# Kernel tuning notes

Measured on AMD Instinct MI355X. Metric: run time of the kernel, lower is better.

Reference implementation:

```python
import jax, jax.numpy as jnp
import numpy as np

H = 16  # number of heads (init kwarg h)

def vdp_matmul(a, va, b, vb):
    # VDP propagation through a matmul of two independent Gaussian tensors:
    # mean = a @ b ; var = va @ vb + va @ b^2 + a^2 @ vb
    mu = jnp.matmul(a, b)
    var = jnp.matmul(va, vb) + jnp.matmul(va, b * b) + jnp.matmul(a * a, vb)
    return mu, var

def softmax_vdp(a, va):
    # diagonal-Jacobian VDP softmax: p = softmax(a); var = (p(1-p))^2 * va
    p = jax.nn.softmax(a, axis=-1)
    return p, (p * (1.0 - p)) ** 2 * va

def setup_inputs() -> dict:
    key = jax.random.key(0)
    ks = jax.random.split(key, 8)
    B, S, D = 2, 1024, 1024
    sc = 1.0 / np.sqrt(D)
    return {
        "x": jax.random.normal(ks[0], (B, S, D), jnp.float32),
        "var_x": jax.random.uniform(ks[1], (B, S, D), jnp.float32) * 0.1,
        "wq_mu": jax.random.normal(ks[2], (D, D), jnp.float32) * sc,
        "wq_var": jax.random.uniform(ks[3], (D, D), jnp.float32) * 0.01,
        "wk_mu": jax.random.normal(ks[4], (D, D), jnp.float32) * sc,
        "wk_var": jax.random.uniform(ks[5], (D, D), jnp.float32) * 0.01,
        "wv_mu": jax.random.normal(ks[6], (D, D), jnp.float32) * sc,
        "wv_var": jax.random.uniform(ks[7], (D, D), jnp.float32) * 0.01,
    }

def _split_heads(t, h):
    B, S, D = t.shape
    return t.reshape(B, S, h, D // h).transpose(0, 2, 1, 3)  # [B,h,S,dh]

def reference(x, var_x, wq_mu, wq_var, wk_mu, wk_var, wv_mu, wv_var):
    D = x.shape[-1]
    rd = jnp.sqrt(jnp.asarray(D, x.dtype))
    # LinearVDP (bias=False): treat weight^T as the second VDP matmul operand
    q, vq = vdp_matmul(x, var_x, wq_mu.T, wq_var.T)
    k, vk = vdp_matmul(x, var_x, wk_mu.T, wk_var.T)
    v, vv = vdp_matmul(x, var_x, wv_mu.T, wv_var.T)
    q, vq = _split_heads(q, H), _split_heads(vq, H)
    k, vk = _split_heads(k, H), _split_heads(vk, H)
    v, vv = _split_heads(v, H), _split_heads(vv, H)
    # scores: q @ k^T with VDP variance, scaled (masking=False path)
    a, va = vdp_matmul(q, vq, k.transpose(0, 1, 3, 2), vk.transpose(0, 1, 3, 2))
    a, va = a / rd, va / (rd * rd)
    a, va = softmax_vdp(a, va)
    # attention-weighted values with VDP variance
    a, va = vdp_matmul(a, va, v, vv)
    a = a.transpose(0, 2, 1, 3).reshape(x.shape)      # [B,S,D]
    va = va.transpose(0, 2, 1, 3).reshape(x.shape)    # [B,S,D]
    return x + a, va
```

## Files before the change

### kernel.cpp

```cpp
#include <hip/hip_runtime.h>
#include <stdint.h>

typedef unsigned short u16;
typedef __attribute__((ext_vector_type(4))) float f32x4;
typedef __attribute__((ext_vector_type(8))) short s16x8;
typedef __attribute__((ext_vector_type(2))) unsigned u32x2;

#define MFMA16(a,b,c) __builtin_amdgcn_mfma_f32_16x16x32_bf16(a,b,c,0,0,0)

__device__ inline u16 f2b(float f){
  unsigned u = __float_as_uint(f);
  unsigned r = u + 0x7fffu + ((u>>16)&1u);
  return (u16)(r>>16);
}
__device__ inline float b2f(u16 b){
  return __uint_as_float(((unsigned)b)<<16);
}
__device__ inline unsigned cvtpk(float lo, float hi){
  unsigned r;
  asm("v_cvt_pk_bf16_f32 %0, %1, %2" : "=v"(r) : "v"(lo), "v"(hi));
  return r;
}
__device__ inline void load_lds16(const void* g, void* l){
  __builtin_amdgcn_global_load_lds((const __attribute__((address_space(1))) void*)g,
                                   (__attribute__((address_space(3))) void*)l, 16, 0, 0);
}

__global__ void prep_in_kernel(const float* __restrict__ x, const float* __restrict__ vx,
                               const float* __restrict__ w0mu, const float* __restrict__ w0va,
                               const float* __restrict__ w1mu, const float* __restrict__ w1va,
                               const float* __restrict__ w2mu, const float* __restrict__ w2va,
                               u16* __restrict__ xb, u16* __restrict__ acat,
                               u16* __restrict__ wmub, u16* __restrict__ bcat){
  int bid = blockIdx.x;
  if (bid < 8192){
    int i = bid*256 + threadIdx.x;
    int j = i & 1023;
    float xv = x[i];
    xb[i] = f2b(xv);
    size_t ar = (size_t)(i >> 10)*2048;
    acat[ar + j]        = f2b(vx[i]);
    acat[ar + 1024 + j] = f2b(xv*xv);
  } else {
    int t = bid - 8192;
    int z = t >> 12;
    int i = (t & 4095)*256 + threadIdx.x;
    const float* wmu = z==0?w0mu:(z==1?w1mu:w2mu);
    const float* wva = z==0?w0va:(z==1?w1va:w2va);
    u16* wb = wmub + (size_t)z*1048576;
    u16* bc = bcat + (size_t)z*2097152;
    int j = i & 1023;
    float mu = wmu[i], va = wva[i];
    wb[i] = f2b(mu);
    size_t br = (size_t)(i >> 10)*2048;
    bc[br + j]        = f2b(va + mu*mu);
    bc[br + 1024 + j] = f2b(va);
  }
}

__global__ __launch_bounds__(256) void gemm_nt6_kernel(
    const u16* __restrict__ xb, const u16* __restrict__ acat,
    const u16* __restrict__ wmub, const u16* __restrict__ bcat,
    u16* __restrict__ cbase){
  int z = blockIdx.z;
  const u16* A = z<3 ? xb : acat;
  int K = z<3 ? 1024 : 2048;
  const u16* B = z<3 ? wmub + (size_t)z*1048576 : bcat + (size_t)(z-3)*2097152;
  u16* C = cbase + (size_t)z*2097152;
  const int N = 1024;
  __shared__ __align__(16) u16 As[2][128*32];
  __shared__ __align__(16) u16 Bs[2][128*32];
  int tid = threadIdx.x;
  int wid = tid>>6, lane = tid&63;
  int wr = wid>>1, wc = wid&1;
  int fr = lane&15, kg = lane>>4;
  int m0 = blockIdx.x*128, n0 = blockIdx.y*128;
  int srow = lane>>2;
  int scol = (lane&3)*8;

  auto stage = [&](int buf, int k0){
    #pragma unroll
    for (int c=0;c<2;c++){
      int r = c*64 + wid*16 + srow;
      load_lds16(A + (size_t)(m0+r)*K + k0 + scol, (char*)As[buf] + (size_t)(c*64+wid*16)*64);
      load_lds16(B + (size_t)(n0+r)*K + k0 + scol, (char*)Bs[buf] + (size_t)(c*64+wid*16)*64);
    }
  };

  f32x4 acc[4][4] = {};
  stage(0, 0);
  __syncthreads();
  int cur = 0;
  for (int k0=0; k0<K; k0+=32){
    if (k0+32<K) stage(cur^1, k0+32);
    s16x8 af[4], bfv[4];
    #pragma unroll
    for (int i=0;i<4;i++){
      af[i]  = *(const s16x8*)(As[cur] + (wr*64 + i*16 + fr)*32 + kg*8);
      bfv[i] = *(const s16x8*)(Bs[cur] + (wc*64 + i*16 + fr)*32 + kg*8);
    }
    #pragma unroll
    for (int i=0;i<4;i++)
      #pragma unroll
      for (int j=0;j<4;j++)
        acc[i][j] = MFMA16(bfv[j], af[i], acc[i][j]);
    __syncthreads();
    cur ^= 1;
  }
  #pragma unroll
  for (int i=0;i<4;i++){
    int mrow = m0 + wr*64 + i*16 + fr;
    #pragma unroll
    for (int j=0;j<4;j++){
      int ncol = n0 + wc*64 + j*16 + kg*4;
      u32x2 pk = {cvtpk(acc[i][j][0],acc[i][j][1]), cvtpk(acc[i][j][2],acc[i][j][3])};
      *(u32x2*)(C + (size_t)mrow*N + ncol) = pk;
    }
  }
}

__global__ void mid_kernel(const u16* __restrict__ kb, const u16* __restrict__ vkb,
                           u16* __restrict__ kw2,
                           const u16* __restrict__ vb, const u16* __restrict__ vvb,
                           u16* __restrict__ vT, u16* __restrict__ vw2T,
                           u16* __restrict__ vvT){
  __shared__ u16 t[32][33];
  int bid = blockIdx.x;
  if (bid < 6144){
    int z = bid / 2048, wI = bid % 2048;
    int bx = wI & 31, by = wI >> 5;
    u16* out = z==0?vT:(z==1?vw2T:vvT);
    int tx = threadIdx.x & 31, ty = threadIdx.x >> 5;
    int c0 = bx*32, r0 = by*32;
    #pragma unroll
    for (int rr=0; rr<32; rr+=8){
      size_t idx = (size_t)(r0+ty+rr)*1024 + c0+tx;
      u16 val;
      if (z==0)      val = vb[idx];
      else if (z==2) val = vvb[idx];
      else {
        float v  = b2f(vb[idx]);
        float vv = b2f(vvb[idx]);
        val = f2b(vv + v*v);
      }
      t[ty+rr][tx] = val;
    }
    __syncthreads();
    #pragma unroll
    for (int rr=0; rr<32; rr+=8)
      out[(size_t)(c0+ty+rr)*2048 + r0+tx] = t[tx][ty+rr];
  } else {
    int i = (bid - 6144)*256 + threadIdx.x;
    float kk = b2f(kb[i]);
    float vk = b2f(vkb[i]);
    kw2[i] = f2b(vk + kk*kk);
  }
}

__global__ __launch_bounds__(256) void attn_vdp_kernel(
  const u16* __restrict__ qb, const u16* __restrict__ vqb,
  const u16* __restrict__ kb, const u16* __restrict__ kw2, const u16* __restrict__ vkb,
  const u16* __restrict__ vT, const u16* __restrict__ vw2T, const u16* __restrict__ vvT,
  const float* __restrict__ x, float* __restrict__ out0, float* __restrict__ out1){
  int qblk = blockIdx.x, h = blockIdx.y, b = blockIdx.z;
  int wid = threadIdx.x>>6, lane = threadIdx.x&63;
  int fr = lane&15, kg = lane>>4;
  int qrow0 = qblk*64 + wid*16;
  size_t mbase = (size_t)b*1024;

  __shared__ __align__(16) u16 bufA[3][4096];
  __shared__ __align__(16) u16 bufB[3][4096];
  __shared__ __align__(16) u16 plds[4][3][16][72];

  const int srow = lane>>3;
  const int sci  = (lane&7) ^ srow;
  const int c0   = wid*2;

  auto stA1 = [&](int jt, u16* dst){
    size_t base = (mbase + (size_t)jt*64)*1024 + h*64;
    #pragma unroll
    for (int c2=0;c2<2;c2++){
      int c = c0+c2;
      size_t go = base + (size_t)(c*8+srow)*1024 + sci*8;
      load_lds16(kb + go, (char*)dst + c*1024);
    }
  };
  auto stK3 = [&](int jt){
    size_t base = (mbase + (size_t)jt*64)*1024 + h*64;
    #pragma unroll
    for (int c2=0;c2<2;c2++){
      int c = c0+c2;
      size_t go = base + (size_t)(c*8+srow)*1024 + sci*8;
      load_lds16(kb  + go, (char*)bufA[0] + c*1024);
      load_lds16(kw2 + go, (char*)bufA[1] + c*1024);
      load_lds16(vkb + go, (char*)bufA[2] + c*1024);
    }
  };
  auto stV3 = [&](int jt){
    size_t base = (size_t)(h*64)*2048 + mbase + (size_t)jt*64;
    #pragma unroll
    for (int c2=0;c2<2;c2++){
      int c = c0+c2;
      size_t go = base + (size_t)(c*8+srow)*2048 + sci*8;
      load_lds16(vT   + go, (char*)bufB[0] + c*1024);
      load_lds16(vw2T + go, (char*)bufB[1] + c*1024);
      load_lds16(vvT  + go, (char*)bufB[2] + c*1024);
    }
  };
  auto frag = [&](const u16* t, int ni, int kf)->s16x8{
    int R = ni*16+fr;
    return *(const s16x8*)(t + R*64 + (((kg + kf*4) ^ (R&7))<<3));
  };

  s16x8 qa[2], vqa[2], qsa[2];
  {
    size_t ro = (mbase + qrow0 + fr)*1024 + h*64 + kg*8;
    #pragma unroll
    for (int kf=0;kf<2;kf++){
      qa[kf]  = *(const s16x8*)(qb  + ro + kf*32);
      vqa[kf] = *(const s16x8*)(vqb + ro + kf*32);
      #pragma unroll
      for (int e=0;e<8;e+=2){
        float lo = b2f((u16)qa[kf][e]);
        float hi = b2f((u16)qa[kf][e+1]);
        unsigned pk = cvtpk(lo*lo, hi*hi);
        qsa[kf][e]   = (short)(pk & 0xffffu);
        qsa[kf][e+1] = (short)(pk >> 16);
      }
    }
  }
  const float scale = 0.03125f;

  float lsum = 0.f;
  stA1(0, bufA[0]);
  __syncthreads();
  for (int jt=0;jt<16;jt++){
    const u16* cur = (jt&1) ? bufB[0] : bufA[0];
    if (jt<15) stA1(jt+1, (jt&1) ? bufA[0] : bufB[0]);
    else       stK3(0);
    f32x4 sacc[4] = {};
    __builtin_amdgcn_s_setprio(1);
    #pragma unroll
    for (int ni=0;ni<4;ni++)
      #pragma unroll
      for (int kf=0;kf<2;kf++)
        sacc[ni] = MFMA16(frag(cur,ni,kf), qa[kf], sacc[ni]);
    __builtin_amdgcn_s_setprio(0);
    #pragma unroll
    for (int ni=0;ni<4;ni++)
      #pragma unroll
      for (int r=0;r<4;r++)
        lsum += __expf(sacc[ni][r]*scale);
    __syncthreads();
  }
  lsum += __shfl_xor(lsum, 16);
  lsum += __shfl_xor(lsum, 32);
  const float linv = 1.f/lsum;

  f32x4 omu[4] = {}, ova[4] = {};
  for (int jt=0;jt<16;jt++){
    stV3(jt);
    f32x4 sacc[4] = {}, vacc[4] = {};
    __builtin_amdgcn_s_setprio(1);
    #pragma unroll
    for (int ni=0;ni<4;ni++)
      #pragma unroll
      for (int kf=0;kf<2;kf++){
        sacc[ni] = MFMA16(frag(bufA[0],ni,kf), qa[kf],  sacc[ni]);
        vacc[ni] = MFMA16(frag(bufA[1],ni,kf), vqa[kf], vacc[ni]);
        vacc[ni] = MFMA16(frag(bufA[2],ni,kf), qsa[kf], vacc[ni]);
      }
    __builtin_amdgcn_s_setprio(0);
    #pragma unroll
    for (int ni=0;ni<4;ni++){
      float pv[4], vpv[4], psv[4];
      #pragma unroll
      for (int r=0;r<4;r++){
        float p  = __expf(sacc[ni][r]*scale) * linv;
        float va = vacc[ni][r] * 9.765625e-4f;
        float g  = p*(1.f-p);
        pv[r]  = p;
        vpv[r] = g*g*va;
        psv[r] = p*p;
      }
      *(u32x2*)&plds[wid][0][fr][ni*16+kg*4] = (u32x2){cvtpk(pv[0],pv[1]),   cvtpk(pv[2],pv[3])};
      *(u32x2*)&plds[wid][1][fr][ni*16+kg*4] = (u32x2){cvtpk(vpv[0],vpv[1]), cvtpk(vpv[2],vpv[3])};
      *(u32x2*)&plds[wid][2][fr][ni*16+kg*4] = (u32x2){cvtpk(psv[0],psv[1]), cvtpk(psv[2],psv[3])};
    }
    s16x8 pa[2], vpa[2], pqa[2];
    #pragma unroll
    for (int kf=0;kf<2;kf++){
      pa[kf]  = *(const s16x8*)&plds[wid][0][fr][kf*32 + kg*8];
      vpa[kf] = *(const s16x8*)&plds[wid][1][fr][kf*32 + kg*8];
      pqa[kf] = *(const s16x8*)&plds[wid][2][fr][kf*32 + kg*8];
    }
    __syncthreads();
    if (jt<15) stK3(jt+1);
    __builtin_amdgcn_s_setprio(1);
    #pragma unroll
    for (int ni=0;ni<4;ni++)
      #pragma unroll
      for (int kf=0;kf<2;kf++){
        omu[ni] = MFMA16(pa[kf],  frag(bufB[0],ni,kf), omu[ni]);
        ova[ni] = MFMA16(vpa[kf], frag(bufB[1],ni,kf), ova[ni]);
        ova[ni] = MFMA16(pqa[kf], frag(bufB[2],ni,kf), ova[ni]);
      }
    __builtin_amdgcn_s_setprio(0);
    __syncthreads();
  }

  #pragma unroll
  for (int ni=0;ni<4;ni++){
    #pragma unroll
    for (int r=0;r<4;r++){
      size_t idx = (mbase + qrow0 + kg*4 + r)*1024 + h*64 + ni*16 + fr;
      out0[idx] = x[idx] + omu[ni][r];
      out1[idx] = ova[ni][r];
    }
  }
}

extern "C" void kernel_launch(void* const* d_in, const int* in_sizes, int n_in,
                              void* d_out, int out_size, void* d_ws, size_t ws_size,
                              hipStream_t stream){
  const float* x    = (const float*)d_in[0];
  const float* vx   = (const float*)d_in[1];
  const float* wqmu = (const float*)d_in[2];
  const float* wqva = (const float*)d_in[3];
  const float* wkmu = (const float*)d_in[4];
  const float* wkva = (const float*)d_in[5];
  const float* wvmu = (const float*)d_in[6];
  const float* wvva = (const float*)d_in[7];
  float* out0 = (float*)d_out;
  float* out1 = out0 + 2u*1024u*1024u;

  char* w = (char*)d_ws;
  const size_t MB = 1024*1024;
  u16* xb   = (u16*)(w +  0*MB);
  u16* acat = (u16*)(w +  4*MB);
  u16* wmub = (u16*)(w + 12*MB);
  u16* bcat = (u16*)(w + 18*MB);
  u16* qb_  = (u16*)(w + 30*MB);
  u16* kb_  = (u16*)(w + 34*MB);
  u16* vb_  = (u16*)(w + 38*MB);
  u16* vqb  = (u16*)(w + 42*MB);
  u16* vkb  = (u16*)(w + 46*MB);
  u16* vvb  = (u16*)(w + 50*MB);
  u16* kw2  = (u16*)(w + 54*MB);
  u16* vT   = (u16*)(w + 58*MB);
  u16* vw2T = (u16*)(w + 62*MB);
  u16* vvT  = (u16*)(w + 66*MB);

  prep_in_kernel<<<20480, 256, 0, stream>>>(x, vx, wqmu, wqva, wkmu, wkva, wvmu, wvva,
                                            xb, acat, wmub, bcat);
  gemm_nt6_kernel<<<dim3(16,8,6), 256, 0, stream>>>(xb, acat, wmub, bcat, qb_);
  mid_kernel<<<14336, 256, 0, stream>>>(kb_, vkb, kw2, vb_, vvb, vT, vw2T, vvT);
  attn_vdp_kernel<<<dim3(16,16,2), 256, 0, stream>>>(qb_, vqb, kb_, kw2, vkb,
                                                     vT, vw2T, vvT, x, out0, out1);
}
```

Baseline: 214.4 us.

## Vectorize prep kernel, triple-buffer GEMM loads, interleave GEMM block order

The prep kernel now has each thread handle four elements with float4 loads and packed bf16 conversions and stores, cutting the thread and instruction count. The projection GEMM moves from double to triple buffering in LDS, with explicit vmcnt waits and a single barrier per k-step, so global-to-LDS loads run two tiles ahead. The GEMM grid is also flattened to 1D with the six GEMMs interleaved per tile position, which changes scheduling and L2 locality and mixes K=1024 and K=2048 blocks. LDS use per block grows by half, which may lower occupancy. The hand-written vmcnt counts depend on the compiler's instruction ordering.

```diff
diff --git a/kernel.cpp b/kernel.cpp
--- a/kernel.cpp
+++ b/kernel.cpp
@@ -33,28 +33,36 @@
                                u16* __restrict__ xb, u16* __restrict__ acat,
                                u16* __restrict__ wmub, u16* __restrict__ bcat){
   int bid = blockIdx.x;
-  if (bid < 8192){
-    int i = bid*256 + threadIdx.x;
-    int j = i & 1023;
-    float xv = x[i];
-    xb[i] = f2b(xv);
-    size_t ar = (size_t)(i >> 10)*2048;
-    acat[ar + j]        = f2b(vx[i]);
-    acat[ar + 1024 + j] = f2b(xv*xv);
+  if (bid < 2048){
+    int i4 = bid*256 + threadIdx.x;
+    int base = i4*4;
+    int j = base & 1023;
+    float4 xv = *(const float4*)(x + base);
+    float4 vv = *(const float4*)(vx + base);
+    u32x2 xpk = {cvtpk(xv.x,xv.y), cvtpk(xv.z,xv.w)};
+    *(u32x2*)(xb + base) = xpk;
+    size_t ar = (size_t)(base >> 10)*2048;
+    *(u32x2*)(acat + ar + j) = (u32x2){cvtpk(vv.x,vv.y), cvtpk(vv.z,vv.w)};
+    *(u32x2*)(acat + ar + 1024 + j) =
+        (u32x2){cvtpk(xv.x*xv.x, xv.y*xv.y), cvtpk(xv.z*xv.z, xv.w*xv.w)};
   } else {
-    int t = bid - 8192;
-    int z = t >> 12;
-    int i = (t & 4095)*256 + threadIdx.x;
+    int t = bid - 2048;
+    int z = t >> 10;
+    int i4 = (t & 1023)*256 + threadIdx.x;
+    int base = i4*4;
     const float* wmu = z==0?w0mu:(z==1?w1mu:w2mu);
     const float* wva = z==0?w0va:(z==1?w1va:w2va);
     u16* wb = wmub + (size_t)z*1048576;
     u16* bc = bcat + (size_t)z*2097152;
-    int j = i & 1023;
-    float mu = wmu[i], va = wva[i];
-    wb[i] = f2b(mu);
-    size_t br = (size_t)(i >> 10)*2048;
-    bc[br + j]        = f2b(va + mu*mu);
-    bc[br + 1024 + j] = f2b(va);
+    int j = base & 1023;
+    float4 mu = *(const float4*)(wmu + base);
+    float4 va = *(const float4*)(wva + base);
+    *(u32x2*)(wb + base) = (u32x2){cvtpk(mu.x,mu.y), cvtpk(mu.z,mu.w)};
+    size_t br = (size_t)(base >> 10)*2048;
+    *(u32x2*)(bc + br + j) =
+        (u32x2){cvtpk(va.x+mu.x*mu.x, va.y+mu.y*mu.y),
+                cvtpk(va.z+mu.z*mu.z, va.w+mu.w*mu.w)};
+    *(u32x2*)(bc + br + 1024 + j) = (u32x2){cvtpk(va.x,va.y), cvtpk(va.z,va.w)};
   }
 }
 
@@ -62,50 +70,57 @@
     const u16* __restrict__ xb, const u16* __restrict__ acat,
     const u16* __restrict__ wmub, const u16* __restrict__ bcat,
     u16* __restrict__ cbase){
-  int z = blockIdx.z;
+  int bid = blockIdx.x;
+  int z = bid % 6;
+  int xy = bid / 6;
+  int bx = xy & 15, by = xy >> 4;
   const u16* A = z<3 ? xb : acat;
   int K = z<3 ? 1024 : 2048;
   const u16* B = z<3 ? wmub + (size_t)z*1048576 : bcat + (size_t)(z-3)*2097152;
   u16* C = cbase + (size_t)z*2097152;
   const int N = 1024;
-  __shared__ __align__(16) u16 As[2][128*32];
-  __shared__ __align__(16) u16 Bs[2][128*32];
+  __shared__ __align__(16) u16 As0[128*32], As1[128*32], As2[128*32];
+  __shared__ __align__(16) u16 Bs0[128*32], Bs1[128*32], Bs2[128*32];
   int tid = threadIdx.x;
   int wid = tid>>6, lane = tid&63;
   int wr = wid>>1, wc = wid&1;
   int fr = lane&15, kg = lane>>4;
-  int m0 = blockIdx.x*128, n0 = blockIdx.y*128;
+  int m0 = bx*128, n0 = by*128;
   int srow = lane>>2;
   int scol = (lane&3)*8;
 
-  auto stage = [&](int buf, int k0){
+  auto stage = [&](u16* Ad, u16* Bd, int k0){
     #pragma unroll
     for (int c=0;c<2;c++){
       int r = c*64 + wid*16 + srow;
-      load_lds16(A + (size_t)(m0+r)*K + k0 + scol, (char*)As[buf] + (size_t)(c*64+wid*16)*64);
-      load_lds16(B + (size_t)(n0+r)*K + k0 + scol, (char*)Bs[buf] + (size_t)(c*64+wid*16)*64);
-    }
-  };
-
+      load_lds16(A + (size_t)(m0+r)*K + k0 + scol, (char*)Ad + (size_t)(c*64+wid*16)*64);
+      load_lds16(B + (size_t)(n0+r)*K + k0 + scol, (char*)Bd + (size_t)(c*64+wid*16)*64);
+    }
+  };
+
+  int nt = K >> 5;
+  u16 *Ar=As0, *An=As1, *At=As2, *Br=Bs0, *Bn=Bs1, *Bt=Bs2;
+  stage(Ar, Br, 0);
+  stage(An, Bn, 32);
   f32x4 acc[4][4] = {};
-  stage(0, 0);
-  __syncthreads();
-  int cur = 0;
-  for (int k0=0; k0<K; k0+=32){
-    if (k0+32<K) stage(cur^1, k0+32);
+  for (int t=0; t<nt; t++){
+    if (t < nt-1) asm volatile("s_waitcnt vmcnt(4)" ::: "memory");
+    else          asm volatile("s_waitcnt vmcnt(0)" ::: "memory");
+    __builtin_amdgcn_s_barrier();
+    if (t+2 < nt) stage(At, Bt, (t+2)*32);
     s16x8 af[4], bfv[4];
     #pragma unroll
     for (int i=0;i<4;i++){
-      af[i]  = *(const s16x8*)(As[cur] + (wr*64 + i*16 + fr)*32 + kg*8);
-      bfv[i] = *(const s16x8*)(Bs[cur] + (wc*64 + i*16 + fr)*32 + kg*8);
+      af[i]  = *(const s16x8*)(Ar + (wr*64 + i*16 + fr)*32 + kg*8);
+      bfv[i] = *(const s16x8*)(Br + (wc*64 + i*16 + fr)*32 + kg*8);
     }
     #pragma unroll
     for (int i=0;i<4;i++)
       #pragma unroll
       for (int j=0;j<4;j++)
         acc[i][j] = MFMA16(bfv[j], af[i], acc[i][j]);
-    __syncthreads();
-    cur ^= 1;
+    u16* ta = Ar; Ar = An; An = At; At = ta;
+    u16* tb = Br; Br = Bn; Bn = Bt; Bt = tb;
   }
   #pragma unroll
   for (int i=0;i<4;i++){
@@ -351,9 +366,9 @@
   u16* vw2T = (u16*)(w + 62*MB);
   u16* vvT  = (u16*)(w + 66*MB);
 
-  prep_in_kernel<<<20480, 256, 0, stream>>>(x, vx, wqmu, wqva, wkmu, wkva, wvmu, wvva,
-                                            xb, acat, wmub, bcat);
-  gemm_nt6_kernel<<<dim3(16,8,6), 256, 0, stream>>>(xb, acat, wmub, bcat, qb_);
+  prep_in_kernel<<<5120, 256, 0, stream>>>(x, vx, wqmu, wqva, wkmu, wkva, wvmu, wvva,
+                                           xb, acat, wmub, bcat);
+  gemm_nt6_kernel<<<768, 256, 0, stream>>>(xb, acat, wmub, bcat, qb_);
   mid_kernel<<<14336, 256, 0, stream>>>(kb_, vkb, kw2, vb_, vvb, vT, vw2T, vvT);
   attn_vdp_kernel<<<dim3(16,16,2), 256, 0, stream>>>(qb_, vqb, kb_, kw2, vkb,
                                                      vT, vw2T, vvT, x, out0, out1);
```

After: 213.8 us. About the same (-0.3%).
